# Kernel tuning notes

Measured on AMD Instinct MI355X. Metric: run time of the kernel, lower is better.

The kernel has to match this reference:

```python
import jax, jax.numpy as jnp
import numpy as np

EMBED_DIM = 1024  # scaling uses embedding_dim**-0.5, as in the source
NEG_INF = -1e9    # keras Softmax masking constant


def setup_inputs() -> dict:
    key = jax.random.key(0)
    k0, k1, k2, k3 = jax.random.split(key, 4)
    B, S, D, H = 8, 2048, 1024, 128
    x = jax.random.normal(k0, (B, S, D), dtype=jnp.float32)
    Wq = jax.random.normal(k1, (D, H), dtype=jnp.float32) * (D ** -0.5)
    Wk = jax.random.normal(k2, (D, H), dtype=jnp.float32) * (D ** -0.5)
    Wv = jax.random.normal(k3, (D, H), dtype=jnp.float32) * (D ** -0.5)
    return {"x": x, "Wq": Wq, "Wk": Wk, "Wv": Wv}


def reference(x, Wq, Wk, Wv):
    # bias-free projections: [B,S,D] @ [D,H] -> [B,S,H]
    q = jnp.einsum("bsd,dh->bsh", x, Wq)
    k = jnp.einsum("bsd,dh->bsh", x, Wk)
    v = jnp.einsum("bsd,dh->bsh", x, Wv)
    # raw scores scaled by embedding_dim**-0.5 (faithful to source)
    w = jnp.einsum("bqh,bkh->bqk", q, k) * (EMBED_DIM ** -0.5)  # [B,S,S]
    # mask = bool(band_part(w, -1, 0)): lower triangle where score != 0
    S = w.shape[-1]
    tril = jnp.tril(jnp.ones((S, S), dtype=bool))
    mask = tril & (w != 0)
    # keras Softmax with mask: add -1e9 where mask is False, then softmax
    w = jnp.where(mask, w, NEG_INF)
    attn = jax.nn.softmax(w, axis=-1)
    return jnp.einsum("bqk,bkh->bqh", attn, v)
```

## Files before the change

### kernel.cpp

```cpp
#include <hip/hip_runtime.h>

typedef short bf8 __attribute__((ext_vector_type(8)));
typedef float f32x4 __attribute__((ext_vector_type(4)));
typedef unsigned short ushort;
typedef unsigned int uint;

#define MFMA16(a, b, c) __builtin_amdgcn_mfma_f32_16x16x32_bf16((a), (b), (c), 0, 0, 0)

static __device__ __forceinline__ ushort f2bf(float f) {
    union { float f; uint u; } v; v.f = f;
    uint u = v.u + 0x7FFFu + ((v.u >> 16) & 1u);
    return (ushort)(u >> 16);
}
static __device__ __forceinline__ float bf2f(ushort u) {
    union { uint u; float f; } v; v.u = ((uint)u) << 16; return v.f;
}
static __device__ __forceinline__ uint pk2(float a, float b) {
    return (uint)f2bf(a) | ((uint)f2bf(b) << 16);
}
static __device__ __forceinline__ void gload16(const void* g, void* l) {
    __builtin_amdgcn_global_load_lds((const __attribute__((address_space(1))) void*)g,
                                     (__attribute__((address_space(3))) void*)l, 16, 0, 0);
}

__global__ __launch_bounds__(256) void k_wconvert(const float* __restrict__ Wq,
                                                  const float* __restrict__ Wk,
                                                  const float* __restrict__ Wv,
                                                  ushort* __restrict__ wT) {
    int idx  = blockIdx.x * 256 + threadIdx.x;
    int proj = idx >> 14;
    int kc   = (idx >> 7) & 127;
    int n    = idx & 127;
    const float* W = (proj == 0) ? Wq : (proj == 1 ? Wk : Wv);
    uint4 w;
    float f[8];
#pragma unroll
    for (int j = 0; j < 8; ++j) f[j] = W[(kc * 8 + j) * 128 + n];
    w.x = pk2(f[0], f[1]); w.y = pk2(f[2], f[3]);
    w.z = pk2(f[4], f[5]); w.w = pk2(f[6], f[7]);
    *(uint4*)&wT[(size_t)proj * 131072 + (size_t)n * 1024 + kc * 8] = w;
}

__global__ __launch_bounds__(256, 3) void k_proj(const float* __restrict__ x,
                                                 const ushort* __restrict__ wT,
                                                 ushort* __restrict__ qb,
                                                 ushort* __restrict__ kb,
                                                 ushort* __restrict__ vT) {
    const int bx = blockIdx.x;
    const int mt = bx & 255;
    const int proj = bx >> 8;
    const int tid = threadIdx.x, lane = tid & 63, wid = tid >> 6;
    const int wm = wid >> 1, wn = wid & 1;
    const int m0 = mt * 64;

    __shared__ __align__(16) ushort sm[64 * 64 + 128 * 64];
    ushort* lA = sm;
    ushort* lB = sm + 64 * 64;

    const ushort* wTp = wT + (size_t)proj * 131072;
    f32x4 acc[2][4] = {};

    const int arow = tid >> 2, aq = tid & 3;
    const float* xrow = x + (size_t)(m0 + arow) * 1024 + aq * 16;

    for (int kt = 0; kt < 1024; kt += 64) {
        __syncthreads();
#pragma unroll
        for (int c = 0; c < 4; ++c) {
            int chunk = tid + 256 * c;
            int n = chunk >> 3, ir = (chunk & 7) * 8;
            const ushort* src = wTp + (size_t)n * 1024 + kt + (ir ^ ((n & 7) << 3));
            ushort* dstb = lB + (size_t)(wid * 64 + 256 * c) * 8;
            gload16(src, dstb);
        }
        {
            const float* xs = xrow + kt;
            float4 a0 = *(const float4*)(xs);
            float4 a1 = *(const float4*)(xs + 4);
            float4 a2 = *(const float4*)(xs + 8);
            float4 a3 = *(const float4*)(xs + 12);
            uint4 w0, w1;
            w0.x = pk2(a0.x, a0.y); w0.y = pk2(a0.z, a0.w);
            w0.z = pk2(a1.x, a1.y); w0.w = pk2(a1.z, a1.w);
            w1.x = pk2(a2.x, a2.y); w1.y = pk2(a2.z, a2.w);
            w1.z = pk2(a3.x, a3.y); w1.w = pk2(a3.z, a3.w);
            const int swz = (arow & 7) << 3;
            const int ir0 = aq * 16;
            *(uint4*)&lA[arow * 64 + (ir0 ^ swz)] = w0;
            *(uint4*)&lA[arow * 64 + ((ir0 + 8) ^ swz)] = w1;
        }
        __syncthreads();

#pragma unroll
        for (int kk = 0; kk < 2; ++kk) {
            const int ir = kk * 32 + (lane >> 4) * 8;
            bf8 a[2], bv[4];
#pragma unroll
            for (int mf = 0; mf < 2; ++mf) {
                int r = wm * 32 + mf * 16 + (lane & 15);
                a[mf] = *(const bf8*)&lA[r * 64 + (ir ^ ((r & 7) << 3))];
            }
#pragma unroll
            for (int nf = 0; nf < 4; ++nf) {
                int r = wn * 64 + nf * 16 + (lane & 15);
                bv[nf] = *(const bf8*)&lB[r * 64 + (ir ^ ((r & 7) << 3))];
            }
#pragma unroll
            for (int mf = 0; mf < 2; ++mf)
#pragma unroll
                for (int nf = 0; nf < 4; ++nf)
                    acc[mf][nf] = MFMA16(a[mf], bv[nf], acc[mf][nf]);
        }
    }
    __syncthreads();

    if (proj < 2) {
        ushort* lT = sm;
#pragma unroll
        for (int mf = 0; mf < 2; ++mf) {
            int row = wm * 32 + mf * 16 + ((lane >> 4) << 2);
#pragma unroll
            for (int nf = 0; nf < 4; ++nf) {
                int col = wn * 64 + nf * 16 + (lane & 15);
#pragma unroll
                for (int i = 0; i < 4; ++i)
                    lT[(row + i) * 136 + col] = f2bf(acc[mf][nf][i]);
            }
        }
        __syncthreads();
        const int row = tid >> 2, seg = (tid & 3) * 32;
        ushort* dst = (proj == 0 ? qb : kb) + (size_t)(m0 + row) * 128 + seg;
        const ushort* srcr = lT + row * 136 + seg;
#pragma unroll
        for (int j = 0; j < 4; ++j)
            *(uint4*)&dst[j * 8] = *(const uint4*)&srcr[j * 8];
    } else {
        ushort* lT = sm;
#pragma unroll
        for (int mf = 0; mf < 2; ++mf) {
            int srow = wm * 32 + mf * 16 + ((lane >> 4) << 2);
#pragma unroll
            for (int nf = 0; nf < 4; ++nf) {
                int h = wn * 64 + nf * 16 + (lane & 15);
#pragma unroll
                for (int i = 0; i < 4; ++i)
                    lT[h * 72 + srow + i] = f2bf(acc[mf][nf][i]);
            }
        }
        __syncthreads();
        const int b = m0 >> 11, s0 = m0 & 2047;
        const int h = tid >> 1, so = (tid & 1) * 32;
        ushort* dst = vT + (size_t)b * 262144 + (size_t)h * 2048 + s0 + so;
#pragma unroll
        for (int j = 0; j < 4; ++j)
            *(uint4*)&dst[j * 8] = *(const uint4*)&lT[h * 72 + so + j * 8];
    }
}

#define NCHUNK 144

__global__ __launch_bounds__(256) void k_attn_part(const ushort* __restrict__ qb,
                                                   const ushort* __restrict__ kb,
                                                   const ushort* __restrict__ vT,
                                                   ushort* __restrict__ pacc,
                                                   float* __restrict__ pml) {
    const int id = blockIdx.x;
    const int b  = id & 7;
    const int cx = id >> 3;
    int g = 0, base = 0;
#pragma unroll
    for (int gg = 0; gg < 8; ++gg) {
        int b0 = 2 * gg * (gg + 1);
        if (cx >= b0) { g = gg; base = b0; }
    }
    const int qt = 4 * g + (cx - base) / (g + 1);
    const int c  = (cx - base) % (g + 1);
    const int kt0 = 4 * c;
    const int kt1 = min(qt + 1, kt0 + 4);

    const int tid = threadIdx.x, lane = tid & 63, wid = tid >> 6;

    __shared__ __align__(16) ushort lK[64 * 128];
    __shared__ __align__(16) ushort lV[128 * 64];
    __shared__ __align__(16) ushort lP[4][16 * 64];

    bf8 qf[4];
    {
        const ushort* qr = qb + (size_t)(b * 2048 + qt * 64 + wid * 16 + (lane & 15)) * 128;
#pragma unroll
        for (int kk = 0; kk < 4; ++kk)
            qf[kk] = *(const bf8*)&qr[kk * 32 + (lane >> 4) * 8];
    }
    bf8 onesf;
#pragma unroll
    for (int j = 0; j < 8; ++j) onesf[j] = (short)0x3F80;

    f32x4 acc[8] = {};
    f32x4 accl = {};
    const int r0 = wid * 16 + ((lane >> 4) << 2);
    const int qg0 = qt * 64 + r0;

    const ushort* kbase = kb + (size_t)b * 2048 * 128;
    const ushort* vbase = vT + (size_t)b * 262144;

    for (int kt = kt0; kt < kt1; ++kt) {
        __syncthreads();
        {
            const ushort* kbt = kbase + (size_t)kt * 64 * 128;
#pragma unroll
            for (int cc = 0; cc < 4; ++cc) {
                int chunk = tid + 256 * cc;
                int r = chunk >> 4, ir = (chunk & 15) * 8;
                gload16(kbt + (size_t)r * 128 + (ir ^ ((r & 7) << 3)),
                        lK + (size_t)(wid * 64 + 256 * cc) * 8);
            }
        }
        {
            const ushort* vbt = vbase + kt * 64;
#pragma unroll
            for (int cc = 0; cc < 4; ++cc) {
                int chunk = tid + 256 * cc;
                int h = chunk >> 3, ir = (chunk & 7) * 8;
                gload16(vbt + (size_t)h * 2048 + (ir ^ ((h & 7) << 3)),
                        lV + (size_t)(wid * 64 + 256 * cc) * 8);
            }
        }
        __syncthreads();

        f32x4 sa[4] = {};
#pragma unroll
        for (int kk = 0; kk < 4; ++kk) {
            const int ir = kk * 32 + (lane >> 4) * 8;
#pragma unroll
            for (int nf = 0; nf < 4; ++nf) {
                int r = nf * 16 + (lane & 15);
                bf8 kf = *(const bf8*)&lK[r * 128 + (ir ^ ((r & 7) << 3))];
                sa[nf] = MFMA16(qf[kk], kf, sa[nf]);
            }
        }

        float p[4][4];
#pragma unroll
        for (int nf = 0; nf < 4; ++nf)
#pragma unroll
            for (int i = 0; i < 4; ++i) {
                float s = sa[nf][i] * 0.03125f;
                if (kt == qt) {
                    int kg = kt * 64 + nf * 16 + (lane & 15);
                    if (kg > qg0 + i) s = -1e30f;
                }
                p[nf][i] = __expf(s);
            }

#pragma unroll
        for (int nf = 0; nf < 4; ++nf)
#pragma unroll
            for (int i = 0; i < 4; ++i) {
                int r = ((lane >> 4) << 2) + i, cp = nf * 16 + (lane & 15);
                lP[wid][r * 64 + (cp ^ ((r & 7) << 3))] = f2bf(p[nf][i]);
            }

#pragma unroll
        for (int kk = 0; kk < 2; ++kk) {
            const int ir = kk * 32 + (lane >> 4) * 8;
            const int pr = lane & 15;
            bf8 pf = *(const bf8*)&lP[wid][pr * 64 + (ir ^ ((pr & 7) << 3))];
            accl = MFMA16(pf, onesf, accl);
#pragma unroll
            for (int nf = 0; nf < 8; ++nf) {
                int h = nf * 16 + (lane & 15);
                bf8 vf = *(const bf8*)&lV[h * 64 + (ir ^ ((h & 7) << 3))];
                acc[nf] = MFMA16(pf, vf, acc[nf]);
            }
        }
    }

    ushort* pa = pacc + ((size_t)(b * NCHUNK + cx) * 64) * 128;
#pragma unroll
    for (int nf = 0; nf < 8; ++nf) {
        int h = nf * 16 + (lane & 15);
#pragma unroll
        for (int i = 0; i < 4; ++i)
            pa[(size_t)(r0 + i) * 128 + h] = f2bf(acc[nf][i]);
    }
    if ((lane & 15) == 0) {
        float* pl = pml + (size_t)(b * NCHUNK + cx) * 64 + r0;
#pragma unroll
        for (int i = 0; i < 4; ++i) pl[i] = accl[i];
    }
}

__global__ __launch_bounds__(256) void k_attn_comb(const ushort* __restrict__ pacc,
                                                   const float* __restrict__ pml,
                                                   float* __restrict__ out) {
    const int qt = blockIdx.x, b = blockIdx.y;
    const int tid = threadIdx.x;
    const int row = tid >> 2, cq = (tid & 3) * 32;
    const int g = qt >> 2;
    const int base = 2 * g * (g + 1) + (qt & 3) * (g + 1);
    const int nch = g + 1;

    float L = 0.f;
    for (int c = 0; c < nch; ++c)
        L += pml[(size_t)(b * NCHUNK + base + c) * 64 + row];
    const float inv = 1.0f / L;

    float s[32] = {};
    for (int c = 0; c < nch; ++c) {
        const ushort* pa = pacc + ((size_t)(b * NCHUNK + base + c) * 64 + row) * 128 + cq;
#pragma unroll
        for (int j = 0; j < 4; ++j) {
            uint4 t = *(const uint4*)&pa[j * 8];
            uint qw[4] = {t.x, t.y, t.z, t.w};
#pragma unroll
            for (int e = 0; e < 4; ++e) {
                s[j * 8 + 2 * e]     += bf2f((ushort)(qw[e] & 0xFFFFu));
                s[j * 8 + 2 * e + 1] += bf2f((ushort)(qw[e] >> 16));
            }
        }
    }
    float* o = out + ((size_t)(b * 2048 + qt * 64 + row)) * 128 + cq;
#pragma unroll
    for (int j = 0; j < 8; ++j) {
        f32x4 v;
#pragma unroll
        for (int e = 0; e < 4; ++e) v[e] = s[j * 4 + e] * inv;
        *(f32x4*)&o[j * 4] = v;
    }
}

extern "C" void kernel_launch(void* const* d_in, const int* in_sizes, int n_in,
                              void* d_out, int out_size, void* d_ws, size_t ws_size,
                              hipStream_t stream) {
    const float* x  = (const float*)d_in[0];
    const float* Wq = (const float*)d_in[1];
    const float* Wk = (const float*)d_in[2];
    const float* Wv = (const float*)d_in[3];
    float* out = (float*)d_out;

    char* ws = (char*)d_ws;
    ushort* qb = (ushort*)(ws);
    ushort* kb = (ushort*)(ws + (4u << 20));
    ushort* vT = (ushort*)(ws + (8u << 20));
    ushort* wT = (ushort*)(ws + (12u << 20));
    float*  pml  = (float*)(ws + (13u << 20));
    ushort* pacc = (ushort*)(ws + (15u << 20));

    k_wconvert<<<192, 256, 0, stream>>>(Wq, Wk, Wv, wT);
    k_proj<<<768, 256, 0, stream>>>(x, wT, qb, kb, vT);
    k_attn_part<<<NCHUNK * 8, 256, 0, stream>>>(qb, kb, vT, pacc, pml);
    k_attn_comb<<<dim3(32, 8), 256, 0, stream>>>(pacc, pml, out);
}
```

Baseline: 68.56 us.

## Double-buffer LDS tiles in projection GEMM to overlap loads with MFMA

```diff
diff --git a/kernel.cpp b/kernel.cpp
--- a/kernel.cpp
+++ b/kernel.cpp
@@ -53,44 +53,35 @@
     const int wm = wid >> 1, wn = wid & 1;
     const int m0 = mt * 64;
 
-    __shared__ __align__(16) ushort sm[64 * 64 + 128 * 64];
-    ushort* lA = sm;
-    ushort* lB = sm + 64 * 64;
+    __shared__ __align__(16) ushort sm[2][64 * 64 + 128 * 64];
 
     const ushort* wTp = wT + (size_t)proj * 131072;
     f32x4 acc[2][4] = {};
 
     const int arow = tid >> 2, aq = tid & 3;
     const float* xrow = x + (size_t)(m0 + arow) * 1024 + aq * 16;
-
-    for (int kt = 0; kt < 1024; kt += 64) {
-        __syncthreads();
+    const int aswz = (arow & 7) << 3;
+    const int air0 = aq * 16;
+
+    auto stageB = [&](int kt, ushort* lB) {
 #pragma unroll
         for (int c = 0; c < 4; ++c) {
             int chunk = tid + 256 * c;
             int n = chunk >> 3, ir = (chunk & 7) * 8;
-            const ushort* src = wTp + (size_t)n * 1024 + kt + (ir ^ ((n & 7) << 3));
-            ushort* dstb = lB + (size_t)(wid * 64 + 256 * c) * 8;
-            gload16(src, dstb);
-        }
-        {
-            const float* xs = xrow + kt;
-            float4 a0 = *(const float4*)(xs);
-            float4 a1 = *(const float4*)(xs + 4);
-            float4 a2 = *(const float4*)(xs + 8);
-            float4 a3 = *(const float4*)(xs + 12);
-            uint4 w0, w1;
-            w0.x = pk2(a0.x, a0.y); w0.y = pk2(a0.z, a0.w);
-            w0.z = pk2(a1.x, a1.y); w0.w = pk2(a1.z, a1.w);
-            w1.x = pk2(a2.x, a2.y); w1.y = pk2(a2.z, a2.w);
-            w1.z = pk2(a3.x, a3.y); w1.w = pk2(a3.z, a3.w);
-            const int swz = (arow & 7) << 3;
-            const int ir0 = aq * 16;
-            *(uint4*)&lA[arow * 64 + (ir0 ^ swz)] = w0;
-            *(uint4*)&lA[arow * 64 + ((ir0 + 8) ^ swz)] = w1;
-        }
-        __syncthreads();
-
+            gload16(wTp + (size_t)n * 1024 + kt + (ir ^ ((n & 7) << 3)),
+                    lB + (size_t)(wid * 64 + 256 * c) * 8);
+        }
+    };
+    auto writeA = [&](ushort* lA, float4 a0, float4 a1, float4 a2, float4 a3) {
+        uint4 w0, w1;
+        w0.x = pk2(a0.x, a0.y); w0.y = pk2(a0.z, a0.w);
+        w0.z = pk2(a1.x, a1.y); w0.w = pk2(a1.z, a1.w);
+        w1.x = pk2(a2.x, a2.y); w1.y = pk2(a2.z, a2.w);
+        w1.z = pk2(a3.x, a3.y); w1.w = pk2(a3.z, a3.w);
+        *(uint4*)&lA[arow * 64 + (air0 ^ aswz)] = w0;
+        *(uint4*)&lA[arow * 64 + ((air0 + 8) ^ aswz)] = w1;
+    };
+    auto compute = [&](const ushort* lA, const ushort* lB) {
 #pragma unroll
         for (int kk = 0; kk < 2; ++kk) {
             const int ir = kk * 32 + (lane >> 4) * 8;
@@ -111,11 +102,37 @@
                 for (int nf = 0; nf < 4; ++nf)
                     acc[mf][nf] = MFMA16(a[mf], bv[nf], acc[mf][nf]);
         }
+    };
+
+    stageB(0, sm[0] + 4096);
+    {
+        float4 a0 = *(const float4*)(xrow);
+        float4 a1 = *(const float4*)(xrow + 4);
+        float4 a2 = *(const float4*)(xrow + 8);
+        float4 a3 = *(const float4*)(xrow + 12);
+        writeA(sm[0], a0, a1, a2, a3);
+    }
+
+    int cur = 0;
+    for (int kt = 0; kt < 15; ++kt) {
+        __syncthreads();
+        ushort* nA = sm[cur ^ 1];
+        stageB((kt + 1) * 64, nA + 4096);
+        const float* xs = xrow + (kt + 1) * 64;
+        float4 a0 = *(const float4*)(xs);
+        float4 a1 = *(const float4*)(xs + 4);
+        float4 a2 = *(const float4*)(xs + 8);
+        float4 a3 = *(const float4*)(xs + 12);
+        compute(sm[cur], sm[cur] + 4096);
+        writeA(nA, a0, a1, a2, a3);
+        cur ^= 1;
     }
     __syncthreads();
+    compute(sm[cur], sm[cur] + 4096);
+    __syncthreads();
 
     if (proj < 2) {
-        ushort* lT = sm;
+        ushort* lT = (ushort*)sm;
 #pragma unroll
         for (int mf = 0; mf < 2; ++mf) {
             int row = wm * 32 + mf * 16 + ((lane >> 4) << 2);
@@ -135,7 +152,7 @@
         for (int j = 0; j < 4; ++j)
             *(uint4*)&dst[j * 8] = *(const uint4*)&srcr[j * 8];
     } else {
-        ushort* lT = sm;
+        ushort* lT = (ushort*)sm;
 #pragma unroll
         for (int mf = 0; mf < 2; ++mf) {
             int srow = wm * 32 + mf * 16 + ((lane >> 4) << 2);
```

After: 69.73 us. About the same (+1.7%).
